# Performance work log

Hardware: AMD Instinct MI355X
Metric: run time of the kernel (lower is better)

## Reference

```python
import jax, jax.numpy as jnp
import numpy as np

D = 256; NHEAD = 8; NQ = 300; NLAYERS = 6; NLEV = 3; NPTS = 4
DFF = 1024; NCLS = 80; BS = 16
SPATIAL = ((80, 80), (40, 40), (20, 20))
LM = sum(h * w for h, w in SPATIAL)
DH = D // NHEAD
PARAM_NAMES = ['sa_wq','sa_bq','sa_wk','sa_bk','sa_wv','sa_bv','sa_wo','sa_bo',
               'ln1_g','ln1_b','ln2_g','ln2_b','ln3_g','ln3_b',
               'off_w','off_b','attw_w','attw_b','val_w','val_b','out_w','out_b',
               'ffn_w1','ffn_b1','ffn_w2','ffn_b2',
               'bb_w1','bb_b1','bb_w2','bb_b2','bb_w3','bb_b3',
               'sc_w','sc_b','qp_w1','qp_b1','qp_w2','qp_b2']


def _ln(x, g, b, eps=1e-5):
    m = x.mean(-1, keepdims=True)
    v = ((x - m) ** 2).mean(-1, keepdims=True)
    return (x - m) * jax.lax.rsqrt(v + eps) * g + b


def _mlp2(x, w1, b1, w2, b2):
    # 2-layer MLP, ReLU on hidden only (act_final_layer=False)
    return jnp.maximum(x @ w1 + b1, 0.0) @ w2 + b2


def _inv_sigmoid(x, eps=1e-5):
    x = jnp.clip(x, 0.0, 1.0)
    return jnp.log(jnp.clip(x, eps, None) / jnp.clip(1.0 - x, eps, None))


def _mha(q, k, v, wq, bq, wk, bk, wv, bv, wo, bo):
    B, N, _ = q.shape
    Q = (q @ wq + bq).reshape(B, N, NHEAD, DH)
    K = (k @ wk + bk).reshape(B, N, NHEAD, DH)
    V = (v @ wv + bv).reshape(B, N, NHEAD, DH)
    att = jnp.einsum('bqhd,bkhd->bhqk', Q, K) * (1.0 / np.sqrt(DH))
    att = jax.nn.softmax(att, axis=-1)
    o = jnp.einsum('bhqk,bkhd->bqhd', att, V).reshape(B, N, D)
    return o @ wo + bo


def _bilinear(v, x, y, Hl, Wl):
    # v: [B, Hl*Wl, C]; x, y: [B, M] pixel coords (align_corners=False, zero padding)
    x0 = jnp.floor(x); y0 = jnp.floor(y)
    wx = x - x0; wy = y - y0
    out = 0.0
    for dx, dy, w in ((0, 0, (1 - wx) * (1 - wy)), (1, 0, wx * (1 - wy)),
                      (0, 1, (1 - wx) * wy), (1, 1, wx * wy)):
        xi = x0 + dx; yi = y0 + dy
        valid = (xi >= 0) & (xi < Wl) & (yi >= 0) & (yi < Hl)
        lin = (jnp.clip(yi, 0, Hl - 1) * Wl + jnp.clip(xi, 0, Wl - 1)).astype(jnp.int32)
        g = jnp.take_along_axis(v, lin[..., None], axis=1)
        out = out + g * (w * valid)[..., None]
    return out


def _deform_attn(q, ref, memory, ow, ob, aw, ab, vw, vb, pw, pb):
    # q: [B,NQ,D]; ref: [B,NQ,4] cxcywh in [0,1]; memory: [B,LM,D]
    B = q.shape[0]
    value = (memory @ vw + vb).reshape(B, LM, NHEAD, DH)
    off = (q @ ow + ob).reshape(B, NQ, NHEAD, NLEV, NPTS, 2)
    attw = jax.nn.softmax((q @ aw + ab).reshape(B, NQ, NHEAD, NLEV * NPTS), -1)
    attw = attw.reshape(B, NQ, NHEAD, NLEV, NPTS)
    r = ref[:, :, None, None, None, :]
    loc = r[..., :2] + off / NPTS * r[..., 2:] * 0.5  # [B,NQ,H,LV,P,2]
    start = 0
    acc = 0.0
    for lv, (Hl, Wl) in enumerate(SPATIAL):
        v = value[:, start:start + Hl * Wl]  # [B, Hl*Wl, H, DH]
        v = v.transpose(0, 2, 1, 3).reshape(B * NHEAD, Hl * Wl, DH)
        g = loc[:, :, :, lv]  # [B,NQ,H,P,2]
        x = (g[..., 0] * Wl - 0.5).transpose(0, 2, 1, 3).reshape(B * NHEAD, NQ * NPTS)
        y = (g[..., 1] * Hl - 0.5).transpose(0, 2, 1, 3).reshape(B * NHEAD, NQ * NPTS)
        s = _bilinear(v, x, y, Hl, Wl).reshape(B, NHEAD, NQ, NPTS, DH)
        w = attw[:, :, :, lv].transpose(0, 2, 1, 3)  # [B,H,NQ,P]
        acc = acc + (s * w[..., None]).sum(3)  # [B,H,NQ,DH]
        start += Hl * Wl
    o = acc.transpose(0, 2, 1, 3).reshape(B, NQ, D)
    return o @ pw + pb


def _decoder(tgt, ref_points_unact, memory, p):
    ref_d = jax.nn.sigmoid(ref_points_unact)
    out = tgt
    for i in range(NLAYERS):
        pos = _mlp2(ref_d, p['qp_w1'], p['qp_b1'], p['qp_w2'], p['qp_b2'])
        q = out + pos
        t2 = _mha(q, q, out, p['sa_wq'][i], p['sa_bq'][i], p['sa_wk'][i], p['sa_bk'][i],
                  p['sa_wv'][i], p['sa_bv'][i], p['sa_wo'][i], p['sa_bo'][i])
        out = _ln(out + t2, p['ln1_g'][i], p['ln1_b'][i])
        t2 = _deform_attn(out + pos, ref_d, memory, p['off_w'][i], p['off_b'][i],
                          p['attw_w'][i], p['attw_b'][i], p['val_w'][i], p['val_b'][i],
                          p['out_w'][i], p['out_b'][i])
        out = _ln(out + t2, p['ln2_g'][i], p['ln2_b'][i])
        out = _ln(out + _mlp2(out, p['ffn_w1'][i], p['ffn_b1'][i], p['ffn_w2'][i], p['ffn_b2'][i]),
                  p['ln3_g'][i], p['ln3_b'][i])
        h = jnp.maximum(out @ p['bb_w1'][i] + p['bb_b1'][i], 0.0)
        h = jnp.maximum(h @ p['bb_w2'][i] + p['bb_b2'][i], 0.0)
        delta = h @ p['bb_w3'][i] + p['bb_b3'][i]
        ref_d = jax.nn.sigmoid(delta + _inv_sigmoid(ref_d))
    logits = out @ p['sc_w'][NLAYERS - 1] + p['sc_b'][NLAYERS - 1]
    return ref_d, logits


def setup_inputs():
    key = jax.random.key(0)
    keys = iter(jax.random.split(key, 64))
    def rn(shape, s=0.02):
        return jax.random.normal(next(keys), shape, jnp.float32) * s
    L = NLAYERS
    inp = {
        'tgt': rn((BS, NQ, D), 1.0),
        'ref_points_unact': rn((BS, NQ, 4), 1.0),
        'memory': rn((BS, LM, D), 1.0),
    }
    for n in ['sa_wq', 'sa_wk', 'sa_wv', 'sa_wo', 'val_w', 'out_w', 'bb_w1', 'bb_w2']:
        inp[n] = rn((L, D, D))
    for n in ['sa_bq', 'sa_bk', 'sa_bv', 'sa_bo', 'ln1_b', 'ln2_b', 'ln3_b',
              'val_b', 'out_b', 'ffn_b2', 'bb_b1', 'bb_b2']:
        inp[n] = jnp.zeros((L, D), jnp.float32)
    for n in ['ln1_g', 'ln2_g', 'ln3_g']:
        inp[n] = jnp.ones((L, D), jnp.float32)
    OFF = NHEAD * NLEV * NPTS * 2
    ATT = NHEAD * NLEV * NPTS
    inp['off_w'] = rn((L, D, OFF)); inp['off_b'] = rn((L, OFF), 0.1)
    inp['attw_w'] = rn((L, D, ATT)); inp['attw_b'] = jnp.zeros((L, ATT), jnp.float32)
    inp['ffn_w1'] = rn((L, D, DFF)); inp['ffn_b1'] = jnp.zeros((L, DFF), jnp.float32)
    inp['ffn_w2'] = rn((L, DFF, D))
    inp['bb_w3'] = rn((L, D, 4)); inp['bb_b3'] = jnp.zeros((L, 4), jnp.float32)
    inp['sc_w'] = rn((L, D, NCLS)); inp['sc_b'] = jnp.zeros((L, NCLS), jnp.float32)
    inp['qp_w1'] = rn((4, 2 * D)); inp['qp_b1'] = jnp.zeros((2 * D,), jnp.float32)
    inp['qp_w2'] = rn((2 * D, D)); inp['qp_b2'] = jnp.zeros((D,), jnp.float32)
    return inp


def reference(tgt, ref_points_unact, memory, sa_wq, sa_bq, sa_wk, sa_bk, sa_wv, sa_bv,
              sa_wo, sa_bo, ln1_g, ln1_b, ln2_g, ln2_b, ln3_g, ln3_b, off_w, off_b,
              attw_w, attw_b, val_w, val_b, out_w, out_b, ffn_w1, ffn_b1, ffn_w2, ffn_b2,
              bb_w1, bb_b1, bb_w2, bb_b2, bb_w3, bb_b3, sc_w, sc_b,
              qp_w1, qp_b1, qp_w2, qp_b2):
    _a = dict(locals())
    p = {k: _a[k] for k in PARAM_NAMES}
    ref_d, logits = _decoder(tgt, ref_points_unact, memory, p)
    # eval path: stacked final-layer outputs, shape [1, BS, NQ, 4] and [1, BS, NQ, NCLS]
    return ref_d[None], logits[None]
```

## Files before the change

kernel.cpp:

```cpp
#include <hip/hip_runtime.h>
#include <hip/hip_bf16.h>

typedef __hip_bfloat16 bf16;
typedef short short8 __attribute__((ext_vector_type(8)));
typedef short short4v __attribute__((ext_vector_type(4)));
typedef float float4v __attribute__((ext_vector_type(4)));

#define D_ 256
#define NHEAD_ 8
#define DH_ 32
#define NQ_ 300
#define NLAYERS_ 6
#define DFF_ 1024
#define NCLS_ 80
#define BS_ 16
#define LM_ 8400
#define BN_ (BS_*NQ_)

static __device__ __forceinline__ short f2bf(float x){
    union{float f; unsigned u;} v; v.f = x;
    unsigned r = v.u + 0x7FFF + ((v.u>>16)&1);
    return (short)(r>>16);
}
static __device__ __forceinline__ float bf2f(short s){
    union{unsigned u; float f;} v; v.u = ((unsigned)(unsigned short)s)<<16; return v.f;
}

__global__ __launch_bounds__(256) void bbox_head_kernel(
    const short* __restrict__ curb,
    const short* __restrict__ w1T, const float* __restrict__ b1,
    const short* __restrict__ w2T, const float* __restrict__ b2,
    const float* __restrict__ w3, const float* __restrict__ b3,
    float* __restrict__ refd)
{
    __shared__ short h1[16*264];
    __shared__ float h2[16*260];
    int m0 = blockIdx.x*16;
    int tid = threadIdx.x, lane = tid&63, wave = tid>>6;
    int lr = lane&15, lq = lane>>4;
    int n0 = wave*64;
    short8 af[8];
    #pragma unroll
    for(int kt=0;kt<8;kt++)
        af[kt] = *(const short8*)(curb + (size_t)(m0+lr)*256 + kt*32 + lq*8);
    float4v acc[4];
    #pragma unroll
    for(int nf=0;nf<4;nf++){ acc[nf].x=0.f; acc[nf].y=0.f; acc[nf].z=0.f; acc[nf].w=0.f; }
    #pragma unroll
    for(int kt=0;kt<8;kt++){
        #pragma unroll
        for(int nf=0;nf<4;nf++){
            short8 bfr = *(const short8*)(w1T + (size_t)(n0+nf*16+lr)*256 + kt*32 + lq*8);
            acc[nf] = __builtin_amdgcn_mfma_f32_16x16x32_bf16(af[kt], bfr, acc[nf], 0,0,0);
        }
    }
    #pragma unroll
    for(int nf=0;nf<4;nf++){
        #pragma unroll
        for(int rr=0;rr<4;rr++){
            int row = lq*4+rr, gn = n0+nf*16+lr;
            float v = acc[nf][rr] + b1[gn];
            v = fmaxf(v,0.f);
            ((bf16*)h1)[row*264+gn] = __float2bfloat16(v);
        }
    }
    __syncthreads();
    #pragma unroll
    for(int nf=0;nf<4;nf++){ acc[nf].x=0.f; acc[nf].y=0.f; acc[nf].z=0.f; acc[nf].w=0.f; }
    #pragma unroll
    for(int kt=0;kt<8;kt++){
        short8 a2 = *(const short8*)(&h1[lr*264 + kt*32 + lq*8]);
        #pragma unroll
        for(int nf=0;nf<4;nf++){
            short8 bfr = *(const short8*)(w2T + (size_t)(n0+nf*16+lr)*256 + kt*32 + lq*8);
            acc[nf] = __builtin_amdgcn_mfma_f32_16x16x32_bf16(a2, bfr, acc[nf], 0,0,0);
        }
    }
    #pragma unroll
    for(int nf=0;nf<4;nf++){
        #pragma unroll
        for(int rr=0;rr<4;rr++){
            int row = lq*4+rr, gn = n0+nf*16+lr;
            float v = acc[nf][rr] + b2[gn];
            h2[row*260+gn] = fmaxf(v,0.f);
        }
    }
    __syncthreads();
    {
        int row = tid>>4, sub = tid&15;
        int n = sub>>2, kq = sub&3;
        float p = 0.f;
        const float* hr = h2 + row*260 + kq*64;
        #pragma unroll
        for(int k=0;k<64;k++) p = fmaf(hr[k], w3[(kq*64+k)*4+n], p);
        p += __shfl_xor(p,1);
        p += __shfl_xor(p,2);
        if(kq==0){
            float delta = p + b3[n];
            size_t idx = (size_t)(m0+row)*4+n;
            float x = refd[idx];
            x = fminf(fmaxf(x,0.f),1.f);
            float num = fmaxf(x,1e-5f), den = fmaxf(1.f-x,1e-5f);
            float nd = delta + logf(num/den);
            refd[idx] = 1.f/(1.f+expf(-nd));
        }
    }
}

__global__ __launch_bounds__(256) void pos_mlp_kernel(
    const float* __restrict__ refd, const float* __restrict__ w1, const float* __restrict__ b1,
    const short* __restrict__ w2T, const float* __restrict__ b2, float* __restrict__ pos)
{
    __shared__ short hs[32*520];
    __shared__ float rs[32*4];
    int n0 = blockIdx.x*64, m0 = blockIdx.y*32;
    int tid = threadIdx.x;
    if(tid<128) rs[tid] = refd[(size_t)m0*4 + tid];
    __syncthreads();
    {
        int c0 = tid&255;
        float w1r[2][4], b1r[2];
        #pragma unroll
        for(int h=0;h<2;h++){
            int c = c0 + h*256;
            b1r[h] = b1[c];
            #pragma unroll
            for(int k=0;k<4;k++) w1r[h][k] = w1[k*512+c];
        }
        #pragma unroll 4
        for(int j=0;j<64;j++){
            int r = j>>1, h = j&1;
            int c = c0 + h*256;
            float v = 0.f;
            #pragma unroll
            for(int k=0;k<4;k++) v = fmaf(rs[r*4+k], w1r[h][k], v);
            v += b1r[h];
            hs[r*520+c] = f2bf(fmaxf(v,0.f));
        }
    }
    __syncthreads();
    int lane = tid&63, wave = tid>>6;
    int wm = (wave>>1)*16, wn = (wave&1)*32;
    int lr = lane&15, lq = lane>>4;
    float4v acc[2];
    #pragma unroll
    for(int j=0;j<2;j++){ acc[j].x=0.f; acc[j].y=0.f; acc[j].z=0.f; acc[j].w=0.f; }
    short8 pb[2][2];
    #pragma unroll
    for(int ni=0;ni<2;ni++)
        pb[0][ni] = *(const short8*)(w2T + (size_t)(n0+wn+ni*16+lr)*512 + lq*8);
    #pragma unroll
    for(int t=0;t<16;t++){
        const int cur = t&1;
        if(t<15){
            #pragma unroll
            for(int ni=0;ni<2;ni++)
                pb[cur^1][ni] = *(const short8*)(w2T + (size_t)(n0+wn+ni*16+lr)*512 + (t+1)*32 + lq*8);
        }
        short8 a0 = *(const short8*)(&hs[(wm+lr)*520 + t*32 + lq*8]);
        acc[0] = __builtin_amdgcn_mfma_f32_16x16x32_bf16(a0, pb[cur][0], acc[0], 0,0,0);
        acc[1] = __builtin_amdgcn_mfma_f32_16x16x32_bf16(a0, pb[cur][1], acc[1], 0,0,0);
    }
    #pragma unroll
    for(int rr=0;rr<4;rr++){
        int gm = m0+wm+lq*4+rr;
        #pragma unroll
        for(int ni=0;ni<2;ni++){
            int gn = n0+wn+ni*16+lr;
            pos[(size_t)gm*256+gn] = acc[ni][rr] + b2[gn];
        }
    }
}

#define LSTR 40

template<int TM, int TN, bool ABF16, bool RELU, bool OUTBF16>
__global__ __launch_bounds__(256) void mfma_gemm_kernel(
    const void* __restrict__ Av, const void* __restrict__ A2v,
    const void* __restrict__ A3v, int nA2lim,
    const short* __restrict__ WT, size_t zWT,
    const float* __restrict__ b0, const float* __restrict__ b1,
    const float* __restrict__ b2, int ns1, int ns2, size_t zB,
    void* __restrict__ Cv, size_t zC, int M, int K, int N, int nxt)
{
    __shared__ short As[2][TM*LSTR];
    __shared__ short Bs[2][TN*LSTR];
    int zz, n0;
    if(nxt){ zz = blockIdx.x / nxt; n0 = (blockIdx.x % nxt)*TN; }
    else   { zz = blockIdx.z;       n0 = blockIdx.x*TN; }
    WT += (size_t)zz*zWT; b0 += (size_t)zz*zB; b1 += (size_t)zz*zB; b2 += (size_t)zz*zB;
    int tid = threadIdx.x;
    int lane = tid&63, wave = tid>>6;
    int m0 = blockIdx.y*TM;
    const int MI = TM/32;
    const int NI = TN/32;
    int wm = (wave>>1)*(TM/2), wn = (wave&1)*(TN/2);
    int lr = lane&15, lq = lane>>4;
    float4v acc[MI][NI];
    #pragma unroll
    for(int i=0;i<MI;i++)
        #pragma unroll
        for(int j=0;j<NI;j++){ acc[i][j].x=0.f; acc[i][j].y=0.f; acc[i][j].z=0.f; acc[i][j].w=0.f; }

    const float* Af; const float* Ad; const short* Ah;
    if(ABF16){ Ah = (const short*)Av; Af=nullptr; Ad=nullptr; }
    else {
        Af = (n0 < nA2lim)? (const float*)Av : (const float*)A3v;
        Ad = (n0 < nA2lim)? (const float*)A2v : nullptr;
        Ah = nullptr;
    }

    short8  rA16[ABF16? TM/64 : 1];
    float4v rAf [ABF16? 1 : TM/32];
    float4v rAd [ABF16? 1 : TM/32];
    short8  rB[TN/64];

    auto LOAD = [&](int k0){
        if constexpr(ABF16){
            #pragma unroll
            for(int it=0; it<TM/64; ++it){
                int idx=(it*256+tid)*8; int r=idx>>5, kk=idx&31; int gm=m0+r;
                short8 v = {};
                if(gm<M) v = *(const short8*)(Ah + (size_t)gm*K + (k0+kk));
                rA16[it]=v;
            }
        } else {
            #pragma unroll
            for(int it=0; it<TM/32; ++it){
                int idx=(it*256+tid)*4; int r=idx>>5, kk=idx&31; int gm=m0+r;
                float4v v; v.x=0.f;v.y=0.f;v.z=0.f;v.w=0.f;
                float4v w; w.x=0.f;w.y=0.f;w.z=0.f;w.w=0.f;
                if(gm<M){
                    v = *(const float4v*)(Af + (size_t)gm*K + (k0+kk));
                    if(Ad) w = *(const float4v*)(Ad + (size_t)gm*K + (k0+kk));
                }
                rAf[it]=v; rAd[it]=w;
            }
        }
        #pragma unroll
        for(int it=0; it<TN/64; ++it){
            int idx=(it*256+tid)*8; int r=idx>>5, kk=idx&31; int gn=n0+r;
            short8 v = {};
            if(gn<N) v = *(const short8*)(WT + (size_t)gn*K + (k0+kk));
            rB[it]=v;
        }
    };
    auto STORE = [&](int buf){
        if constexpr(ABF16){
            #pragma unroll
            for(int it=0; it<TM/64; ++it){
                int idx=(it*256+tid)*8; int r=idx>>5, kk=idx&31;
                *(short8*)(&As[buf][r*LSTR+kk]) = rA16[it];
            }
        } else {
            #pragma unroll
            for(int it=0; it<TM/32; ++it){
                int idx=(it*256+tid)*4; int r=idx>>5, kk=idx&31;
                float4v v = rAf[it];
                if(Ad){ v.x+=rAd[it].x; v.y+=rAd[it].y; v.z+=rAd[it].z; v.w+=rAd[it].w; }
                short4v h; h.x=f2bf(v.x); h.y=f2bf(v.y); h.z=f2bf(v.z); h.w=f2bf(v.w);
                *(short4v*)(&As[buf][r*LSTR+kk]) = h;
            }
        }
        #pragma unroll
        for(int it=0; it<TN/64; ++it){
            int idx=(it*256+tid)*8; int r=idx>>5, kk=idx&31;
            *(short8*)(&Bs[buf][r*LSTR+kk]) = rB[it];
        }
    };

    const int nt = K>>5;
    LOAD(0);
    STORE(0);
    __syncthreads();
    for(int t=0; t<nt; ++t){
        int cb = t&1;
        if(t+1<nt) LOAD((t+1)<<5);
        short8 af[MI], bfr[NI];
        #pragma unroll
        for(int mi=0;mi<MI;mi++) af[mi]  = *(const short8*)(&As[cb][(wm+mi*16+lr)*LSTR + lq*8]);
        #pragma unroll
        for(int ni=0;ni<NI;ni++) bfr[ni] = *(const short8*)(&Bs[cb][(wn+ni*16+lr)*LSTR + lq*8]);
        #pragma unroll
        for(int mi=0;mi<MI;mi++)
            #pragma unroll
            for(int ni=0;ni<NI;ni++)
                acc[mi][ni] = __builtin_amdgcn_mfma_f32_16x16x32_bf16(af[mi], bfr[ni], acc[mi][ni], 0,0,0);
        if(t+1<nt){
            STORE(cb^1);
            __syncthreads();
        }
    }
    float* Cf=(float*)Cv + (size_t)zz*zC; bf16* Ch=(bf16*)Cv + (size_t)zz*zC;
    #pragma unroll
    for(int mi=0;mi<MI;mi++){
        #pragma unroll
        for(int r=0;r<4;r++){
            int gm = m0+wm+mi*16+lq*4+r;
            if(gm>=M) continue;
            #pragma unroll
            for(int ni=0;ni<NI;ni++){
                int gn = n0+wn+ni*16+lr;
                if(gn>=N) continue;
                float bv = (gn<ns1)? b0[gn] : ((gn<ns2)? b1[gn-ns1] : b2[gn-ns2]);
                float v = acc[mi][ni][r] + bv;
                if(RELU) v = fmaxf(v,0.f);
                if(OUTBF16) Ch[(size_t)gm*N+gn]=__float2bfloat16(v);
                else        Cf[(size_t)gm*N+gn]=v;
            }
        }
    }
}

__global__ __launch_bounds__(256) void fused_mha_kernel(
    const float* __restrict__ QKV, short* __restrict__ O)
{
    const int ld = 768;
    int bh = blockIdx.y; int b = bh>>3, h = bh&7;
    int q0 = blockIdx.x*64;
    __shared__ short lds[31104];
    short* Vts = lds;
    short* Qs  = lds + 10368;
    short* Ks  = lds + 12672;
    short* Ps  = lds + 10368;
    int tid = threadIdx.x;
    for(int idx=tid; idx<64*8; idx+=256){
        int r=idx>>3, c4=(idx&7)*4; int gq=q0+r;
        float4v v; v.x=0.f;v.y=0.f;v.z=0.f;v.w=0.f;
        if(gq<NQ_) v = *(const float4v*)(QKV + ((size_t)(b*NQ_+gq))*ld + h*DH_ + c4);
        short4v h4; h4.x=f2bf(v.x);h4.y=f2bf(v.y);h4.z=f2bf(v.z);h4.w=f2bf(v.w);
        *(short4v*)(Qs + r*36 + c4) = h4;
    }
    for(int idx=tid; idx<304*8; idx+=256){
        int r=idx>>3, c4=(idx&7)*4;
        float4v v; v.x=0.f;v.y=0.f;v.z=0.f;v.w=0.f;
        if(r<NQ_) v = *(const float4v*)(QKV + 256 + ((size_t)(b*NQ_+r))*ld + h*DH_ + c4);
        short4v h4; h4.x=f2bf(v.x);h4.y=f2bf(v.y);h4.z=f2bf(v.z);h4.w=f2bf(v.w);
        *(short4v*)(Ks + r*36 + c4) = h4;
    }
    for(int idx=tid; idx<320*8; idx+=256){
        int r=idx>>3, c4=(idx&7)*4;
        float4v v; v.x=0.f;v.y=0.f;v.z=0.f;v.w=0.f;
        if(r<NQ_) v = *(const float4v*)(QKV + 512 + ((size_t)(b*NQ_+r))*ld + h*DH_ + c4);
        Vts[(c4+0)*324+r]=f2bf(v.x); Vts[(c4+1)*324+r]=f2bf(v.y);
        Vts[(c4+2)*324+r]=f2bf(v.z); Vts[(c4+3)*324+r]=f2bf(v.w);
    }
    __syncthreads();

    int lane = tid&63, wave = tid>>6;
    int lr = lane&15, lq = lane>>4;
    int mrow = wave*16;
    const float scale = 0.17677669529663687f;

    float4v acc[19];
    #pragma unroll
    for(int t=0;t<19;t++){ acc[t].x=0.f; acc[t].y=0.f; acc[t].z=0.f; acc[t].w=0.f; }
    short8 afrag = *(const short8*)(&Qs[(mrow+lr)*36 + lq*8]);
    #pragma unroll
    for(int t=0;t<19;t++){
        short8 bfrag = *(const short8*)(&Ks[(t*16+lr)*36 + lq*8]);
        acc[t] = __builtin_amdgcn_mfma_f32_16x16x32_bf16(afrag, bfrag, acc[t], 0,0,0);
    }
    __syncthreads();

    for(int idx=tid; idx<64*16; idx+=256){
        int r=idx>>4, c=idx&15;
        Ps[r*324 + 304 + c]=0;
    }
    #pragma unroll
    for(int t=0;t<19;t++){
        #pragma unroll
        for(int r=0;r<4;r++) acc[t][r] *= scale;
    }
    if(lr>=12){
        #pragma unroll
        for(int r=0;r<4;r++) acc[18][r] = -1e30f;
    }
    float mx[4];
    #pragma unroll
    for(int r=0;r<4;r++){
        float m = acc[0][r];
        #pragma unroll
        for(int t=1;t<19;t++) m = fmaxf(m, acc[t][r]);
        m = fmaxf(m, __shfl_xor(m,1)); m = fmaxf(m, __shfl_xor(m,2));
        m = fmaxf(m, __shfl_xor(m,4)); m = fmaxf(m, __shfl_xor(m,8));
        mx[r]=m;
    }
    float sum[4] = {0.f,0.f,0.f,0.f};
    #pragma unroll
    for(int t=0;t<19;t++){
        #pragma unroll
        for(int r=0;r<4;r++){
            float p = __expf(acc[t][r]-mx[r]);
            acc[t][r]=p; sum[r]+=p;
        }
    }
    #pragma unroll
    for(int r=0;r<4;r++){
        float s = sum[r];
        s += __shfl_xor(s,1); s += __shfl_xor(s,2);
        s += __shfl_xor(s,4); s += __shfl_xor(s,8);
        sum[r] = 1.f/s;
    }
    #pragma unroll
    for(int t=0;t<19;t++){
        #pragma unroll
        for(int r=0;r<4;r++){
            Ps[(mrow + lq*4 + r)*324 + t*16 + lr] = f2bf(acc[t][r]*sum[r]);
        }
    }
    __syncthreads();
    float4v oacc[2];
    oacc[0].x=0.f;oacc[0].y=0.f;oacc[0].z=0.f;oacc[0].w=0.f;
    oacc[1]=oacc[0];
    #pragma unroll
    for(int kc=0;kc<10;kc++){
        short8 pa = *(const short8*)(&Ps[(mrow+lr)*324 + kc*32 + lq*8]);
        #pragma unroll
        for(int n=0;n<2;n++){
            short8 vb = *(const short8*)(&Vts[(n*16+lr)*324 + kc*32 + lq*8]);
            oacc[n] = __builtin_amdgcn_mfma_f32_16x16x32_bf16(pa, vb, oacc[n], 0,0,0);
        }
    }
    #pragma unroll
    for(int n=0;n<2;n++){
        #pragma unroll
        for(int r=0;r<4;r++){
            int gq = q0 + mrow + lq*4 + r;
            if(gq<NQ_)
                O[((size_t)(b*NQ_+gq))*D_ + h*DH_ + n*16 + lr] = f2bf(oacc[n][r]);
        }
    }
}

#define NTD 74
struct TD { const float* src; unsigned dstoff; int K, N, base; };
struct TAll { TD d[NTD]; };

__global__ __launch_bounds__(256) void transpose_all_kernel(TAll p, short* __restrict__ WTb){
    int blk = blockIdx.x;
    int di = 0;
    #pragma unroll 1
    for(int i=0;i<NTD;i++){ if(blk >= p.d[i].base) di = i; }
    TD d = p.d[di];
    int rel = blk - d.base;
    int ntx = (d.N+31)/32;
    int tn = (rel % ntx)*32, tk = (rel / ntx)*32;
    __shared__ float t[32][33];
    int tx = threadIdx.x&31, ty = threadIdx.x>>5;
    for(int i=0;i<32;i+=8){
        int k = tk+ty+i, n = tn+tx;
        t[ty+i][tx] = (k<d.K && n<d.N)? d.src[(size_t)k*d.N+n] : 0.f;
    }
    __syncthreads();
    short* out = WTb + d.dstoff;
    for(int i=0;i<32;i+=8){
        int n = tn+ty+i, k = tk+tx;
        if(n<d.N && k<d.K) out[(size_t)n*d.K+k] = f2bf(t[tx][ty+i]);
    }
}

__global__ void copy_kernel(const float* __restrict__ a, float* __restrict__ o, int n){
    int i = blockIdx.x*blockDim.x+threadIdx.x;
    if(i<n) o[i]=a[i];
}
__global__ void cvt_f32_bf16_kernel(const float* __restrict__ a, short* __restrict__ o, int n4){
    int i = blockIdx.x*blockDim.x+threadIdx.x;
    if(i<n4){
        float4v v = *(const float4v*)(a + (size_t)i*4);
        short4v h; h.x=f2bf(v.x); h.y=f2bf(v.y); h.z=f2bf(v.z); h.w=f2bf(v.w);
        *(short4v*)(o + (size_t)i*4) = h;
    }
}
__global__ void sigmoid_init_kernel(const float* __restrict__ a, float* __restrict__ o, int n){
    int i = blockIdx.x*blockDim.x+threadIdx.x;
    if(i<n){ float x=a[i]; o[i]=1.f/(1.f+expf(-x)); }
}
__global__ void write_out_kernel(const float* __restrict__ refd, const float* __restrict__ logits, float* __restrict__ out){
    int i = blockIdx.x*blockDim.x+threadIdx.x;
    if(i<BN_*4) out[i]=refd[i];
    else if(i<BN_*4+BN_*NCLS_) out[i]=logits[i-BN_*4];
}

__global__ __launch_bounds__(256) void ln_residual_kernel(
    float* __restrict__ cur, const short* __restrict__ t2b,
    const float* __restrict__ g, const float* __restrict__ b,
    short* __restrict__ cb)
{
    int row = blockIdx.x; int c = threadIdx.x;
    size_t idx = (size_t)row*D_+c;
    float x = cur[idx] + bf2f(t2b[idx]);
    float v1 = x, v2 = x*x;
    #pragma unroll
    for(int o=32;o>0;o>>=1){ v1 += __shfl_down(v1,o,64); v2 += __shfl_down(v2,o,64); }
    __shared__ float s1[4], s2[4], st[2];
    int wid=c>>6, lane=c&63;
    if(lane==0){ s1[wid]=v1; s2[wid]=v2; }
    __syncthreads();
    if(c==0){
        float a=0,d=0;
        #pragma unroll
        for(int i=0;i<4;i++){a+=s1[i]; d+=s2[i];}
        st[0]=a/(float)D_; st[1]=d/(float)D_;
    }
    __syncthreads();
    float m=st[0], var=st[1]-m*m;
    float y = (x-m)*rsqrtf(var+1e-5f)*g[c] + b[c];
    cur[idx]=y;
    if(cb) cb[idx]=f2bf(y);
}

__global__ __launch_bounds__(256) void deform_sample_kernel(
    const float* __restrict__ refd, const float* __restrict__ oab,
    const bf16* __restrict__ value, short* __restrict__ outacc)
{
    int row = blockIdx.x; int b = row/NQ_;
    int tid = threadIdx.x; int h = tid>>5, c = tid&31;
    __shared__ float so[192], sa[96], sr[4];
    if(tid<192) so[tid]=oab[(size_t)row*288+tid];
    if(tid<96)  sa[tid]=oab[(size_t)row*288+192+tid];
    if(tid<4)   sr[tid]=refd[(size_t)row*4+tid];
    __syncthreads();
    if(tid<8){
        float* p = sa + tid*12;
        float m=-1e30f;
        #pragma unroll
        for(int i2=0;i2<12;i2++) m=fmaxf(m,p[i2]);
        float s=0.f;
        #pragma unroll
        for(int i2=0;i2<12;i2++){ float e=__expf(p[i2]-m); p[i2]=e; s+=e; }
        float inv=1.f/s;
        #pragma unroll
        for(int i2=0;i2<12;i2++) p[i2]*=inv;
    }
    __syncthreads();
    float cx=sr[0], cy=sr[1], rw=sr[2], rh=sr[3];
    const int HS[3]={80,40,20}, WS[3]={80,40,20}, ST[3]={0,6400,8000};
    float acc=0.f;
    const bf16* vb = value + (size_t)b*LM_*D_ + h*DH_ + c;
    for(int lv=0;lv<3;lv++){
        int Hl=HS[lv], Wl=WS[lv], st=ST[lv];
        #pragma unroll
        for(int pt=0;pt<4;pt++){
            int oi = ((h*3+lv)*4+pt)*2;
            float ox=so[oi], oy=so[oi+1];
            float wa=sa[h*12+lv*4+pt];
            float lx = cx + ox*0.25f*rw*0.5f;
            float ly = cy + oy*0.25f*rh*0.5f;
            float x = lx*(float)Wl - 0.5f, y = ly*(float)Hl - 0.5f;
            float x0f=floorf(x), y0f=floorf(y);
            float wx=x-x0f, wy=y-y0f;
            int x0=(int)x0f, y0=(int)y0f;
            #pragma unroll
            for(int dy=0;dy<2;dy++){
                #pragma unroll
                for(int dx=0;dx<2;dx++){
                    int xi=x0+dx, yi=y0+dy;
                    if(xi>=0 && xi<Wl && yi>=0 && yi<Hl){
                        float w = (dx? wx : 1.f-wx)*(dy? wy : 1.f-wy);
                        int lin = yi*Wl+xi;
                        acc += __bfloat162float(vb[(size_t)(st+lin)*D_]) * (w*wa);
                    }
                }
            }
        }
    }
    outacc[(size_t)row*D_+tid]=f2bf(acc);
}

static void g64x(const void*A, const void*A2, const void*A3, int nA2lim,
                 const short*WT, const float*b0, const float*b1, const float*b2,
                 int ns1, int ns2, void*C, int M,int K,int N,
                 bool abf16, bool relu, bool outbf, hipStream_t s){
    dim3 g((N+63)/64,(M+63)/64,1);
    #define CALLG(AB,RL,OB) mfma_gemm_kernel<64,64,AB,RL,OB><<<g,256,0,s>>>(A,A2,A3,nA2lim,WT,0,b0,b1,b2,ns1,ns2,0,C,0,M,K,N,0)
    if(abf16){
        if(relu){ if(outbf) CALLG(true,true,true);  else CALLG(true,true,false); }
        else    { if(outbf) CALLG(true,false,true); else CALLG(true,false,false); }
    } else {
        if(relu){ if(outbf) CALLG(false,true,true);  else CALLG(false,true,false); }
        else    { if(outbf) CALLG(false,false,true); else CALLG(false,false,false); }
    }
    #undef CALLG
}
static void g64(const float*A, const float*A2, const float*A3, int nA2lim,
                const short*WT, const float*b0, const float*b1, const float*b2,
                int ns1, int ns2, void*C, int M,int K,int N,
                bool relu, bool outbf, hipStream_t s){
    g64x(A,A2,A3,nA2lim,WT,b0,b1,b2,ns1,ns2,C,M,K,N,false,relu,outbf,s);
}
static void g64b(const short*A, const short*WT, const float*b, void*C,
                 int M,int K,int N, hipStream_t s){
    g64x(A,nullptr,nullptr,1<<30,WT,b,b,b,N,N+1,C,M,K,N,true,false,true,s);
}
static int ntiles(int K,int N){ return ((N+31)/32)*((K+31)/32); }

extern "C" void kernel_launch(void* const* d_in, const int* in_sizes, int n_in,
                              void* d_out, int out_size, void* d_ws, size_t ws_size,
                              hipStream_t stream) {
    const float* tgt   = (const float*)d_in[0];
    const float* rpu   = (const float*)d_in[1];
    const float* mem   = (const float*)d_in[2];
    const float* sa_wq = (const float*)d_in[3];
    const float* sa_wk = (const float*)d_in[4];
    const float* sa_wv = (const float*)d_in[5];
    const float* sa_wo = (const float*)d_in[6];
    const float* val_w = (const float*)d_in[7];
    const float* out_w = (const float*)d_in[8];
    const float* bb_w1 = (const float*)d_in[9];
    const float* bb_w2 = (const float*)d_in[10];
    const float* sa_bq = (const float*)d_in[11];
    const float* sa_bk = (const float*)d_in[12];
    const float* sa_bv = (const float*)d_in[13];
    const float* sa_bo = (const float*)d_in[14];
    const float* ln1_b = (const float*)d_in[15];
    const float* ln2_b = (const float*)d_in[16];
    const float* ln3_b = (const float*)d_in[17];
    const float* val_b = (const float*)d_in[18];
    const float* out_b = (const float*)d_in[19];
    const float* ffn_b2= (const float*)d_in[20];
    const float* bb_b1 = (const float*)d_in[21];
    const float* bb_b2 = (const float*)d_in[22];
    const float* ln1_g = (const float*)d_in[23];
    const float* ln2_g = (const float*)d_in[24];
    const float* ln3_g = (const float*)d_in[25];
    const float* off_w = (const float*)d_in[26];
    const float* off_b = (const float*)d_in[27];
    const float* attw_w= (const float*)d_in[28];
    const float* attw_b= (const float*)d_in[29];
    const float* ffn_w1= (const float*)d_in[30];
    const float* ffn_b1= (const float*)d_in[31];
    const float* ffn_w2= (const float*)d_in[32];
    const float* bb_w3 = (const float*)d_in[33];
    const float* bb_b3 = (const float*)d_in[34];
    const float* sc_w  = (const float*)d_in[35];
    const float* sc_b  = (const float*)d_in[36];
    const float* qp_w1 = (const float*)d_in[37];
    const float* qp_b1 = (const float*)d_in[38];
    const float* qp_w2 = (const float*)d_in[39];
    const float* qp_b2 = (const float*)d_in[40];

    const size_t BND = (size_t)BN_*D_;
    const size_t USZ = (size_t)BN_*DFF_;
    const size_t LMD = (size_t)BS_*LM_*D_;
    const size_t LSZ = 1122304;

    float* ws   = (float*)d_ws;
    float* cur  = ws;
    float* pos  = cur + BND;
    float* refd = pos + BND;
    float* U    = refd + (size_t)BN_*4;
    short* tmp16 = (short*)(U + USZ);
    short* t216  = tmp16 + BND;
    short* WT    = t216 + BND;
    short* qp2T  = WT + 6*LSZ;
    short* scT   = qp2T + 131072;
    short* X     = scT + 20480;
    float* QKVh   = U;
    float* offsb  = U;
    short* ffnh16 = (short*)U;
    float* logitsb= U;
    short* curb = tmp16;

    size_t offX = (size_t)((char*)X - (char*)d_ws);
    int vmode;
    if(ws_size >= offX + 7*LMD*2)      vmode = 3;
    else if(ws_size >= offX + 6*LMD*2) vmode = 2;
    else if(ws_size >= offX + 4*LMD)   vmode = 1;
    else                               vmode = 0;
    short* memT   = X;
    short* values = (vmode==3)? X + LMD : X;
    short* value1 = X + LMD;
    short* value0 = X;

    const int nBN_D = (int)BND;
    copy_kernel<<<(nBN_D+255)/256,256,0,stream>>>(tgt, cur, nBN_D);
    sigmoid_init_kernel<<<(BN_*4+255)/256,256,0,stream>>>(rpu, refd, BN_*4);
    if(vmode==1 || vmode==3){
        int n4 = (int)(LMD/4);
        cvt_f32_bf16_kernel<<<(n4+255)/256,256,0,stream>>>(mem, memT, n4);
    }

    {
        TAll tp; int base=0; int di=0;
        const size_t offs[12] = { 0,65536,131072,196608,262144,327680,
                                  393216,442368,466944,729088,991232,1056768 };
        const int Ks[12] = { 256,256,256,256,256,256,256,256,256,1024,256,256 };
        const int Ns[12] = { 256,256,256,256,256,256,192,96,1024,256,256,256 };
        for(int l=0;l<NLAYERS_;l++){
            const float* srcs[12] = { sa_wq+(size_t)l*D_*D_, sa_wk+(size_t)l*D_*D_, sa_wv+(size_t)l*D_*D_,
                                      sa_wo+(size_t)l*D_*D_, val_w+(size_t)l*D_*D_, out_w+(size_t)l*D_*D_,
                                      off_w+(size_t)l*D_*192, attw_w+(size_t)l*D_*96,
                                      ffn_w1+(size_t)l*D_*DFF_, ffn_w2+(size_t)l*DFF_*D_,
                                      bb_w1+(size_t)l*D_*D_, bb_w2+(size_t)l*D_*D_ };
            for(int j=0;j<12;j++){
                tp.d[di] = { srcs[j], (unsigned)(l*LSZ + offs[j]), Ks[j], Ns[j], base };
                base += ntiles(Ks[j],Ns[j]); di++;
            }
        }
        tp.d[di] = { qp_w2, (unsigned)(6*LSZ), 512, 256, base }; base += ntiles(512,256); di++;
        tp.d[di] = { sc_w + (size_t)(NLAYERS_-1)*D_*NCLS_, (unsigned)(6*LSZ+131072), 256, 80, base }; base += ntiles(256,80); di++;
        transpose_all_kernel<<<base,256,0,stream>>>(tp, WT);
    }

    if(vmode==3){
        dim3 g(12,1050,1);
        mfma_gemm_kernel<128,128,true,false,true><<<g,256,0,stream>>>(
            memT,nullptr,nullptr,1<<30, WT+262144, LSZ,
            val_b,val_b,val_b, 256,257, 256, values, LMD, BS_*LM_, D_, D_, 2);
    } else if(vmode==2){
        dim3 g(12,1050,1);
        mfma_gemm_kernel<128,128,false,false,true><<<g,256,0,stream>>>(
            mem,nullptr,mem,1<<30, WT+262144, LSZ,
            val_b,val_b,val_b, 256,257, 256, values, LMD, BS_*LM_, D_, D_, 2);
    }

    for(int i=0;i<NLAYERS_;i++){
        const bf16* value_i;
        if(vmode>=2) value_i = (const bf16*)(values + (size_t)i*LMD);
        else {
            dim3 g(2,1050,1);
            if(vmode==1){
                mfma_gemm_kernel<128,128,true,false,true><<<g,256,0,stream>>>(
                    memT,nullptr,nullptr,1<<30, WT+i*LSZ+262144, 0,
                    val_b+(size_t)i*D_,val_b,val_b, 256,257, 0, value1, 0, BS_*LM_, D_, D_, 0);
                value_i = (const bf16*)value1;
            } else {
                mfma_gemm_kernel<128,128,false,false,true><<<g,256,0,stream>>>(
                    mem,nullptr,mem,1<<30, WT+i*LSZ+262144, 0,
                    val_b+(size_t)i*D_,val_b,val_b, 256,257, 0, value0, 0, BS_*LM_, D_, D_, 0);
                value_i = (const bf16*)value0;
            }
        }
        pos_mlp_kernel<<<dim3(4,150),256,0,stream>>>(refd, qp_w1, qp_b1, qp2T, qp_b2, pos);
        g64(cur, pos, cur, 512, WT+i*LSZ,
            sa_bq+(size_t)i*D_, sa_bk+(size_t)i*D_, sa_bv+(size_t)i*D_, 256, 512,
            QKVh, BN_, D_, 768, false,false, stream);
        {
            dim3 g((NQ_+63)/64, BS_*NHEAD_);
            fused_mha_kernel<<<g,256,0,stream>>>(QKVh, tmp16);
        }
        g64b(tmp16, WT+i*LSZ+196608, sa_bo+(size_t)i*D_, t216, BN_, D_, D_, stream);
        ln_residual_kernel<<<BN_,256,0,stream>>>(cur, t216, ln1_g+(size_t)i*D_, ln1_b+(size_t)i*D_, nullptr);
        g64(cur, pos, cur, 1<<30, WT+i*LSZ+393216,
            off_b+(size_t)i*192, attw_b+(size_t)i*96, attw_b+(size_t)i*96, 192, 288,
            offsb, BN_, D_, 288, false,false, stream);
        deform_sample_kernel<<<BN_,256,0,stream>>>(refd, offsb, value_i, tmp16);
        g64b(tmp16, WT+i*LSZ+327680, out_b+(size_t)i*D_, t216, BN_, D_, D_, stream);
        ln_residual_kernel<<<BN_,256,0,stream>>>(cur, t216, ln2_g+(size_t)i*D_, ln2_b+(size_t)i*D_, curb);
        g64x(curb,nullptr,nullptr,1<<30, WT+i*LSZ+466944, ffn_b1+(size_t)i*DFF_,ffn_b1,ffn_b1, DFF_,DFF_+1,
             ffnh16, BN_, D_, DFF_, true,true,true, stream);
        g64x(ffnh16,nullptr,nullptr,1<<30, WT+i*LSZ+729088, ffn_b2+(size_t)i*D_,ffn_b2,ffn_b2, 256,257,
             t216, BN_, DFF_, D_, true,false,true, stream);
        ln_residual_kernel<<<BN_,256,0,stream>>>(cur, t216, ln3_g+(size_t)i*D_, ln3_b+(size_t)i*D_, curb);
        bbox_head_kernel<<<BN_/16,256,0,stream>>>(curb,
            WT+i*LSZ+991232, bb_b1+(size_t)i*D_,
            WT+i*LSZ+1056768, bb_b2+(size_t)i*D_,
            bb_w3+(size_t)i*D_*4, bb_b3+(size_t)i*4, refd);
    }
    g64x(curb,nullptr,nullptr,1<<30, scT, sc_b+(size_t)(NLAYERS_-1)*NCLS_,sc_b,sc_b, NCLS_,NCLS_+1,
         logitsb, BN_, D_, NCLS_, true,false,false, stream);
    int tot = BN_*4 + BN_*NCLS_;
    write_out_kernel<<<(tot+255)/256,256,0,stream>>>(refd, logitsb, (float*)d_out);
}
```

Measured before the change: 2.167 ms.

## Feed QKV and offset GEMMs with precomputed bf16 inputs and bf16 QKV output

Measured after the change: 2.072 ms. 4.4% less time.

```diff
diff --git a/kernel.cpp b/kernel.cpp
--- a/kernel.cpp
+++ b/kernel.cpp
@@ -109,7 +109,8 @@
 
 __global__ __launch_bounds__(256) void pos_mlp_kernel(
     const float* __restrict__ refd, const float* __restrict__ w1, const float* __restrict__ b1,
-    const short* __restrict__ w2T, const float* __restrict__ b2, float* __restrict__ pos)
+    const short* __restrict__ w2T, const float* __restrict__ b2,
+    const float* __restrict__ cur, float* __restrict__ pos, short* __restrict__ qpb)
 {
     __shared__ short hs[32*520];
     __shared__ float rs[32*4];
@@ -151,15 +152,15 @@
         pb[0][ni] = *(const short8*)(w2T + (size_t)(n0+wn+ni*16+lr)*512 + lq*8);
     #pragma unroll
     for(int t=0;t<16;t++){
-        const int cur = t&1;
+        const int cur2 = t&1;
         if(t<15){
             #pragma unroll
             for(int ni=0;ni<2;ni++)
-                pb[cur^1][ni] = *(const short8*)(w2T + (size_t)(n0+wn+ni*16+lr)*512 + (t+1)*32 + lq*8);
+                pb[cur2^1][ni] = *(const short8*)(w2T + (size_t)(n0+wn+ni*16+lr)*512 + (t+1)*32 + lq*8);
         }
         short8 a0 = *(const short8*)(&hs[(wm+lr)*520 + t*32 + lq*8]);
-        acc[0] = __builtin_amdgcn_mfma_f32_16x16x32_bf16(a0, pb[cur][0], acc[0], 0,0,0);
-        acc[1] = __builtin_amdgcn_mfma_f32_16x16x32_bf16(a0, pb[cur][1], acc[1], 0,0,0);
+        acc[0] = __builtin_amdgcn_mfma_f32_16x16x32_bf16(a0, pb[cur2][0], acc[0], 0,0,0);
+        acc[1] = __builtin_amdgcn_mfma_f32_16x16x32_bf16(a0, pb[cur2][1], acc[1], 0,0,0);
     }
     #pragma unroll
     for(int rr=0;rr<4;rr++){
@@ -167,7 +168,10 @@
         #pragma unroll
         for(int ni=0;ni<2;ni++){
             int gn = n0+wn+ni*16+lr;
-            pos[(size_t)gm*256+gn] = acc[ni][rr] + b2[gn];
+            size_t idx = (size_t)gm*256+gn;
+            float p = acc[ni][rr] + b2[gn];
+            pos[idx] = p;
+            qpb[idx] = f2bf(cur[idx] + p);
         }
     }
 }
@@ -203,8 +207,10 @@
         for(int j=0;j<NI;j++){ acc[i][j].x=0.f; acc[i][j].y=0.f; acc[i][j].z=0.f; acc[i][j].w=0.f; }
 
     const float* Af; const float* Ad; const short* Ah;
-    if(ABF16){ Ah = (const short*)Av; Af=nullptr; Ad=nullptr; }
-    else {
+    if(ABF16){
+        Ah = (n0 < nA2lim)? (const short*)Av : (const short*)A3v;
+        Af=nullptr; Ad=nullptr;
+    } else {
         Af = (n0 < nA2lim)? (const float*)Av : (const float*)A3v;
         Ad = (n0 < nA2lim)? (const float*)A2v : nullptr;
         Ah = nullptr;
@@ -313,7 +319,7 @@
 }
 
 __global__ __launch_bounds__(256) void fused_mha_kernel(
-    const float* __restrict__ QKV, short* __restrict__ O)
+    const short* __restrict__ QKV, short* __restrict__ O)
 {
     const int ld = 768;
     int bh = blockIdx.y; int b = bh>>3, h = bh&7;
@@ -324,26 +330,24 @@
     short* Ks  = lds + 12672;
     short* Ps  = lds + 10368;
     int tid = threadIdx.x;
-    for(int idx=tid; idx<64*8; idx+=256){
-        int r=idx>>3, c4=(idx&7)*4; int gq=q0+r;
-        float4v v; v.x=0.f;v.y=0.f;v.z=0.f;v.w=0.f;
-        if(gq<NQ_) v = *(const float4v*)(QKV + ((size_t)(b*NQ_+gq))*ld + h*DH_ + c4);
-        short4v h4; h4.x=f2bf(v.x);h4.y=f2bf(v.y);h4.z=f2bf(v.z);h4.w=f2bf(v.w);
-        *(short4v*)(Qs + r*36 + c4) = h4;
-    }
-    for(int idx=tid; idx<304*8; idx+=256){
-        int r=idx>>3, c4=(idx&7)*4;
-        float4v v; v.x=0.f;v.y=0.f;v.z=0.f;v.w=0.f;
-        if(r<NQ_) v = *(const float4v*)(QKV + 256 + ((size_t)(b*NQ_+r))*ld + h*DH_ + c4);
-        short4v h4; h4.x=f2bf(v.x);h4.y=f2bf(v.y);h4.z=f2bf(v.z);h4.w=f2bf(v.w);
-        *(short4v*)(Ks + r*36 + c4) = h4;
-    }
-    for(int idx=tid; idx<320*8; idx+=256){
-        int r=idx>>3, c4=(idx&7)*4;
-        float4v v; v.x=0.f;v.y=0.f;v.z=0.f;v.w=0.f;
-        if(r<NQ_) v = *(const float4v*)(QKV + 512 + ((size_t)(b*NQ_+r))*ld + h*DH_ + c4);
-        Vts[(c4+0)*324+r]=f2bf(v.x); Vts[(c4+1)*324+r]=f2bf(v.y);
-        Vts[(c4+2)*324+r]=f2bf(v.z); Vts[(c4+3)*324+r]=f2bf(v.w);
+    for(int idx=tid; idx<64*4; idx+=256){
+        int r=idx>>2, c8=(idx&3)*8; int gq=q0+r;
+        short8 v = {};
+        if(gq<NQ_) v = *(const short8*)(QKV + (size_t)(b*NQ_+gq)*ld + h*DH_ + c8);
+        *(short8*)(Qs + r*36 + c8) = v;
+    }
+    for(int idx=tid; idx<304*4; idx+=256){
+        int r=idx>>2, c8=(idx&3)*8;
+        short8 v = {};
+        if(r<NQ_) v = *(const short8*)(QKV + 256 + (size_t)(b*NQ_+r)*ld + h*DH_ + c8);
+        *(short8*)(Ks + r*36 + c8) = v;
+    }
+    for(int idx=tid; idx<320*4; idx+=256){
+        int r=idx>>2, c8=(idx&3)*8;
+        short8 v = {};
+        if(r<NQ_) v = *(const short8*)(QKV + 512 + (size_t)(b*NQ_+r)*ld + h*DH_ + c8);
+        #pragma unroll
+        for(int j=0;j<8;j++) Vts[(c8+j)*324+r] = v[j];
     }
     __syncthreads();
 
@@ -460,9 +464,10 @@
     }
 }
 
-__global__ void copy_kernel(const float* __restrict__ a, float* __restrict__ o, int n){
+__global__ void copy_kernel(const float* __restrict__ a, float* __restrict__ o,
+                            short* __restrict__ cb, int n){
     int i = blockIdx.x*blockDim.x+threadIdx.x;
-    if(i<n) o[i]=a[i];
+    if(i<n){ float v=a[i]; o[i]=v; cb[i]=f2bf(v); }
 }
 __global__ void cvt_f32_bf16_kernel(const float* __restrict__ a, short* __restrict__ o, int n4){
     int i = blockIdx.x*blockDim.x+threadIdx.x;
@@ -485,7 +490,7 @@
 __global__ __launch_bounds__(256) void ln_residual_kernel(
     float* __restrict__ cur, const short* __restrict__ t2b,
     const float* __restrict__ g, const float* __restrict__ b,
-    short* __restrict__ cb)
+    short* __restrict__ cb, const float* __restrict__ pa)
 {
     int row = blockIdx.x; int c = threadIdx.x;
     size_t idx = (size_t)row*D_+c;
@@ -507,7 +512,7 @@
     float m=st[0], var=st[1]-m*m;
     float y = (x-m)*rsqrtf(var+1e-5f)*g[c] + b[c];
     cur[idx]=y;
-    if(cb) cb[idx]=f2bf(y);
+    if(cb) cb[idx] = f2bf(pa? y + pa[idx] : y);
 }
 
 __global__ __launch_bounds__(256) void deform_sample_kernel(
@@ -583,15 +588,9 @@
     }
     #undef CALLG
 }
-static void g64(const float*A, const float*A2, const float*A3, int nA2lim,
-                const short*WT, const float*b0, const float*b1, const float*b2,
-                int ns1, int ns2, void*C, int M,int K,int N,
-                bool relu, bool outbf, hipStream_t s){
-    g64x(A,A2,A3,nA2lim,WT,b0,b1,b2,ns1,ns2,C,M,K,N,false,relu,outbf,s);
-}
 static void g64b(const short*A, const short*WT, const float*b, void*C,
                  int M,int K,int N, hipStream_t s){
-    g64x(A,nullptr,nullptr,1<<30,WT,b,b,b,N,N+1,C,M,K,N,true,false,true,s);
+    g64x(A,nullptr,A,1<<30,WT,b,b,b,N,N+1,C,M,K,N,true,false,true,s);
 }
 static int ntiles(int K,int N){ return ((N+31)/32)*((K+31)/32); }
 
@@ -655,8 +654,9 @@
     short* WT    = t216 + BND;
     short* qp2T  = WT + 6*LSZ;
     short* scT   = qp2T + 131072;
-    short* X     = scT + 20480;
-    float* QKVh   = U;
+    short* qpb   = scT + 20480;
+    short* X     = qpb + BND;
+    short* QKVh16 = (short*)U;
     float* offsb  = U;
     short* ffnh16 = (short*)U;
     float* logitsb= U;
@@ -674,7 +674,7 @@
     short* value0 = X;
 
     const int nBN_D = (int)BND;
-    copy_kernel<<<(nBN_D+255)/256,256,0,stream>>>(tgt, cur, nBN_D);
+    copy_kernel<<<(nBN_D+255)/256,256,0,stream>>>(tgt, cur, curb, nBN_D);
     sigmoid_init_kernel<<<(BN_*4+255)/256,256,0,stream>>>(rpu, refd, BN_*4);
     if(vmode==1 || vmode==3){
         int n4 = (int)(LMD/4);
@@ -706,7 +706,7 @@
     if(vmode==3){
         dim3 g(12,1050,1);
         mfma_gemm_kernel<128,128,true,false,true><<<g,256,0,stream>>>(
-            memT,nullptr,nullptr,1<<30, WT+262144, LSZ,
+            memT,nullptr,memT,1<<30, WT+262144, LSZ,
             val_b,val_b,val_b, 256,257, 256, values, LMD, BS_*LM_, D_, D_, 2);
     } else if(vmode==2){
         dim3 g(12,1050,1);
@@ -722,7 +722,7 @@
             dim3 g(2,1050,1);
             if(vmode==1){
                 mfma_gemm_kernel<128,128,true,false,true><<<g,256,0,stream>>>(
-                    memT,nullptr,nullptr,1<<30, WT+i*LSZ+262144, 0,
+                    memT,nullptr,memT,1<<30, WT+i*LSZ+262144, 0,
                     val_b+(size_t)i*D_,val_b,val_b, 256,257, 0, value1, 0, BS_*LM_, D_, D_, 0);
                 value_i = (const bf16*)value1;
             } else {
@@ -732,33 +732,34 @@
                 value_i = (const bf16*)value0;
             }
         }
-        pos_mlp_kernel<<<dim3(4,150),256,0,stream>>>(refd, qp_w1, qp_b1, qp2T, qp_b2, pos);
-        g64(cur, pos, cur, 512, WT+i*LSZ,
-            sa_bq+(size_t)i*D_, sa_bk+(size_t)i*D_, sa_bv+(size_t)i*D_, 256, 512,
-            QKVh, BN_, D_, 768, false,false, stream);
+        pos_mlp_kernel<<<dim3(4,150),256,0,stream>>>(refd, qp_w1, qp_b1, qp2T, qp_b2,
+                                                     cur, pos, qpb);
+        g64x(qpb, nullptr, curb, 512, WT+i*LSZ,
+             sa_bq+(size_t)i*D_, sa_bk+(size_t)i*D_, sa_bv+(size_t)i*D_, 256, 512,
+             QKVh16, BN_, D_, 768, true,false,true, stream);
         {
             dim3 g((NQ_+63)/64, BS_*NHEAD_);
-            fused_mha_kernel<<<g,256,0,stream>>>(QKVh, tmp16);
+            fused_mha_kernel<<<g,256,0,stream>>>(QKVh16, tmp16);
         }
         g64b(tmp16, WT+i*LSZ+196608, sa_bo+(size_t)i*D_, t216, BN_, D_, D_, stream);
-        ln_residual_kernel<<<BN_,256,0,stream>>>(cur, t216, ln1_g+(size_t)i*D_, ln1_b+(size_t)i*D_, nullptr);
-        g64(cur, pos, cur, 1<<30, WT+i*LSZ+393216,
-            off_b+(size_t)i*192, attw_b+(size_t)i*96, attw_b+(size_t)i*96, 192, 288,
-            offsb, BN_, D_, 288, false,false, stream);
+        ln_residual_kernel<<<BN_,256,0,stream>>>(cur, t216, ln1_g+(size_t)i*D_, ln1_b+(size_t)i*D_, qpb, pos);
+        g64x(qpb, nullptr, qpb, 1<<30, WT+i*LSZ+393216,
+             off_b+(size_t)i*192, attw_b+(size_t)i*96, attw_b+(size_t)i*96, 192, 288,
+             offsb, BN_, D_, 288, true,false,false, stream);
         deform_sample_kernel<<<BN_,256,0,stream>>>(refd, offsb, value_i, tmp16);
         g64b(tmp16, WT+i*LSZ+327680, out_b+(size_t)i*D_, t216, BN_, D_, D_, stream);
-        ln_residual_kernel<<<BN_,256,0,stream>>>(cur, t216, ln2_g+(size_t)i*D_, ln2_b+(size_t)i*D_, curb);
-        g64x(curb,nullptr,nullptr,1<<30, WT+i*LSZ+466944, ffn_b1+(size_t)i*DFF_,ffn_b1,ffn_b1, DFF_,DFF_+1,
+        ln_residual_kernel<<<BN_,256,0,stream>>>(cur, t216, ln2_g+(size_t)i*D_, ln2_b+(size_t)i*D_, curb, nullptr);
+        g64x(curb,nullptr,curb,1<<30, WT+i*LSZ+466944, ffn_b1+(size_t)i*DFF_,ffn_b1,ffn_b1, DFF_,DFF_+1,
              ffnh16, BN_, D_, DFF_, true,true,true, stream);
-        g64x(ffnh16,nullptr,nullptr,1<<30, WT+i*LSZ+729088, ffn_b2+(size_t)i*D_,ffn_b2,ffn_b2, 256,257,
+        g64x(ffnh16,nullptr,ffnh16,1<<30, WT+i*LSZ+729088, ffn_b2+(size_t)i*D_,ffn_b2,ffn_b2, 256,257,
              t216, BN_, DFF_, D_, true,false,true, stream);
-        ln_residual_kernel<<<BN_,256,0,stream>>>(cur, t216, ln3_g+(size_t)i*D_, ln3_b+(size_t)i*D_, curb);
+        ln_residual_kernel<<<BN_,256,0,stream>>>(cur, t216, ln3_g+(size_t)i*D_, ln3_b+(size_t)i*D_, curb, nullptr);
         bbox_head_kernel<<<BN_/16,256,0,stream>>>(curb,
             WT+i*LSZ+991232, bb_b1+(size_t)i*D_,
             WT+i*LSZ+1056768, bb_b2+(size_t)i*D_,
             bb_w3+(size_t)i*D_*4, bb_b3+(size_t)i*4, refd);
     }
-    g64x(curb,nullptr,nullptr,1<<30, scT, sc_b+(size_t)(NLAYERS_-1)*NCLS_,sc_b,sc_b, NCLS_,NCLS_+1,
+    g64x(curb,nullptr,curb,1<<30, scT, sc_b+(size_t)(NLAYERS_-1)*NCLS_,sc_b,sc_b, NCLS_,NCLS_+1,
          logitsb, BN_, D_, NCLS_, true,false,false, stream);
     int tot = BN_*4 + BN_*NCLS_;
     write_out_kernel<<<(tot+255)/256,256,0,stream>>>(refd, logitsb, (float*)d_out);
```
